# Kernel optimization log

Measured on AMD Instinct MI355X. Metric: run time of the kernel, lower is better.

## Reference

```python
import jax, jax.numpy as jnp
from jax import lax
import numpy as np

MAX_FLARES = 6
NMS_KERNEL = 9
CONF_THRESHOLD = 0.3


def setup_inputs() -> dict:
    key = jax.random.key(0)
    heatmap = jax.random.uniform(key, (64, 1, 640, 640), dtype=jnp.float32)
    return {"heatmap": heatmap}


def reference(heatmap):
    # heatmap: [B, 1, H, W]
    B, _, H, W = heatmap.shape
    K = MAX_FLARES
    hm = heatmap[:, 0]  # [B, H, W]

    # NMS via max-pool: kernel NMS_KERNEL, stride 1, SAME padding (pad = k//2)
    hm_max = lax.reduce_window(
        hm, -jnp.inf, lax.max,
        window_dimensions=(1, NMS_KERNEL, NMS_KERNEL),
        window_strides=(1, 1, 1),
        padding="SAME",
    )
    peaks = (hm == hm_max) & (hm > CONF_THRESHOLD)  # [B, H, W] bool
    scores = jnp.where(peaks, hm, jnp.float32(0.0))  # suppressed -> 0

    # Batched top-K over flattened spatial dims (replaces per-batch Python loop)
    flat = scores.reshape(B, H * W)
    top_scores, top_idx = lax.top_k(flat, K)  # [B, K] each, sorted desc

    # A slot is valid iff its score is a true peak (> threshold). Since all
    # non-peak entries were zeroed, this exactly reproduces the original's
    # min(K, n_peaks) truncation + `break` on sub-threshold scores.
    valid = top_scores > CONF_THRESHOLD  # [B, K]

    xs_grid = jnp.linspace(0.0, 1.0, W, dtype=hm.dtype)
    ys_grid = jnp.linspace(0.0, 1.0, H, dtype=hm.dtype)
    x_idx = top_idx % W
    y_idx = top_idx // W

    pos_x = jnp.where(valid, xs_grid[x_idx], jnp.float32(-1.0))
    pos_y = jnp.where(valid, ys_grid[y_idx], jnp.float32(-1.0))
    pred_positions = jnp.stack([pos_x, pos_y], axis=-1)  # [B, K, 2]
    pred_conf = jnp.where(valid, top_scores, jnp.float32(0.0))  # [B, K]
    return pred_positions, pred_conf
```

## Files before the change

### kernel.cpp

```cpp
#include <hip/hip_runtime.h>
#include <float.h>

#define HH 640
#define WW 640
#define KTOP 6
#define CONF 0.3f
#define NTHR 256
#define XBANDS 3
#define XOUT 248
#define SEG 40
#define CHUNK 8
#define NITER (SEG / CHUNK)
#define YSEGS (HH / SEG)
#define TASKS_PER_B (XBANDS * YSEGS)
#define MENT (TASKS_PER_B * KTOP)
#define CAP 256

__device__ __forceinline__ float4 f4max(float4 a, float4 b) {
    return make_float4(fmaxf(a.x, b.x), fmaxf(a.y, b.y), fmaxf(a.z, b.z), fmaxf(a.w, b.w));
}

__global__ __launch_bounds__(NTHR) void peaks_kernel(const float* __restrict__ hm,
                                                     float* __restrict__ bscore,
                                                     int* __restrict__ bidx) {
    __shared__ float c_score[4][CAP];
    __shared__ int   c_idx[4][CAP];
    __shared__ int   c_cnt[4];

    const int t    = threadIdx.x;
    const int lane = t & 63;
    const int w    = t >> 6;
    const int task = blockIdx.x * 4 + w;
    const int b    = task / TASKS_PER_B;
    const int rem  = task - b * TASKS_PER_B;
    const int ys   = rem / XBANDS;
    const int xb   = rem - ys * XBANDS;
    const int ybase = ys * SEG;
    const int x_raw = xb * XOUT - 4 + 4 * lane;
    const int xc    = min(max(x_raw, 0), WW - 4);
    const bool xok  = (x_raw >= 0) && (x_raw <= WW - 4);
    const bool vlane = (lane >= 1) && (lane <= 62) && xok;
    const float* colp = hm + (size_t)b * (HH * WW) + xc;
    const float4 NEG = make_float4(-FLT_MAX, -FLT_MAX, -FLT_MAX, -FLT_MAX);

    if (lane == 0) c_cnt[w] = 0;
    __syncthreads();

    #define LDC(dst, yy) { int gy = (yy); \
        gy = gy < 0 ? 0 : (gy > HH - 1 ? HH - 1 : gy); \
        dst = *reinterpret_cast<const float4*>(colp + (size_t)gy * WW); }

    #define PROCROW(m, c, gy_) { \
        const float w0 = __shfl_up(m.x, 1),  w1 = __shfl_up(m.y, 1); \
        const float w2 = __shfl_up(m.z, 1),  w3 = __shfl_up(m.w, 1); \
        const float w8 = __shfl_down(m.x, 1), w9 = __shfl_down(m.y, 1); \
        const float wA = __shfl_down(m.z, 1), wB = __shfl_down(m.w, 1); \
        const float hc = fmaxf(fmaxf(fmaxf(w3, m.x), fmaxf(m.y, m.z)), fmaxf(m.w, w8)); \
        const float ha = fmaxf(w1, w2); \
        const float hb = fmaxf(w9, wA); \
        const float h0 = fmaxf(hc, fmaxf(w0, ha)); \
        const float h1 = fmaxf(hc, fmaxf(ha, w9)); \
        const float h2 = fmaxf(hc, fmaxf(w2, hb)); \
        const float h3 = fmaxf(hc, fmaxf(hb, wB)); \
        if (vlane) { \
            const int base = (gy_) * WW + x_raw; \
            if (c.x > CONF && c.x >= h0) { int p_ = atomicAdd(&c_cnt[w], 1); if (p_ < CAP) { c_score[w][p_] = c.x; c_idx[w][p_] = base;     } } \
            if (c.y > CONF && c.y >= h1) { int p_ = atomicAdd(&c_cnt[w], 1); if (p_ < CAP) { c_score[w][p_] = c.y; c_idx[w][p_] = base + 1; } } \
            if (c.z > CONF && c.z >= h2) { int p_ = atomicAdd(&c_cnt[w], 1); if (p_ < CAP) { c_score[w][p_] = c.z; c_idx[w][p_] = base + 2; } } \
            if (c.w > CONF && c.w >= h3) { int p_ = atomicAdd(&c_cnt[w], 1); if (p_ < CAP) { c_score[w][p_] = c.w; c_idx[w][p_] = base + 3; } } \
        } \
    }

    float4 p[8], n[8], f[8];
    #pragma unroll
    for (int i = 0; i < 8; ++i) LDC(p[i], ybase - 4 + i)
    #pragma unroll
    for (int i = 0; i < 8; ++i) LDC(n[i], ybase + 4 + i)

    #pragma unroll
    for (int k = 0; k < NITER; ++k) {
        const int R = ybase + CHUNK * k;
        if (k < NITER - 1) {
            #pragma unroll
            for (int i = 0; i < 8; ++i) LDC(f[i], R + 12 + i)
        }
        float4 S[8];
        S[7] = p[7];
        #pragma unroll
        for (int i = 6; i >= 0; --i) S[i] = f4max(p[i], S[i + 1]);
        float4 pref = n[0];
        #pragma unroll
        for (int i = 0; i < 8; ++i) {
            if (i > 0) pref = f4max(pref, n[i]);
            float4 m = f4max(S[i], pref);
            if (!xok) m = NEG;
            const float4 c = (i < 4) ? p[4 + i] : n[i - 4];
            PROCROW(m, c, R + i)
        }
        if (k < NITER - 1) {
            #pragma unroll
            for (int i = 0; i < 8; ++i) { p[i] = n[i]; n[i] = f[i]; }
        }
    }

    {
        const int cnt = min(c_cnt[w], CAP);
        float cs[4]; int ci[4];
        #pragma unroll
        for (int j = 0; j < 4; ++j) {
            const int pos = lane + 64 * j;
            const bool ok = pos < cnt;
            cs[j] = ok ? c_score[w][pos] : -2.0f;
            ci[j] = ok ? c_idx[w][pos]   : 0x7fffffff;
        }
        const int outbase = task * KTOP;
        #pragma unroll
        for (int k = 0; k < KTOP; ++k) {
            float bs = cs[0]; int bi = ci[0];
            #pragma unroll
            for (int j = 1; j < 4; ++j)
                if (cs[j] > bs || (cs[j] == bs && ci[j] < bi)) { bs = cs[j]; bi = ci[j]; }
            #pragma unroll
            for (int off = 32; off >= 1; off >>= 1) {
                const float os = __shfl_xor(bs, off);
                const int   oi = __shfl_xor(bi, off);
                if (os > bs || (os == bs && oi < bi)) { bs = os; bi = oi; }
            }
            if (lane == 0) { bscore[outbase + k] = bs; bidx[outbase + k] = bi; }
            #pragma unroll
            for (int j = 0; j < 4; ++j) if (ci[j] == bi) cs[j] = -3.0f;
        }
    }
}

__global__ __launch_bounds__(64) void topk_kernel(const float* __restrict__ bscore,
                                                  const int* __restrict__ bidx,
                                                  float* __restrict__ out,
                                                  int B) {
    const int t = threadIdx.x;
    const int b = blockIdx.x;

    float s[5]; int id5[5];
    #pragma unroll
    for (int j = 0; j < 5; ++j) {
        const int e = t + 64 * j;
        const bool ok = e < MENT;
        s[j]   = ok ? bscore[b * MENT + e] : -9.0f;
        id5[j] = ok ? bidx[b * MENT + e]   : 0x7fffffff;
    }

    float my_s = -9.0f; int my_i = 0x7fffffff;
    #pragma unroll
    for (int k = 0; k < KTOP; ++k) {
        float bs = s[0]; int bi = id5[0];
        #pragma unroll
        for (int j = 1; j < 5; ++j)
            if (s[j] > bs || (s[j] == bs && id5[j] < bi)) { bs = s[j]; bi = id5[j]; }
        #pragma unroll
        for (int off = 32; off >= 1; off >>= 1) {
            const float os = __shfl_xor(bs, off);
            const int   oi = __shfl_xor(bi, off);
            if (os > bs || (os == bs && oi < bi)) { bs = os; bi = oi; }
        }
        if (t == k) { my_s = bs; my_i = bi; }
        #pragma unroll
        for (int j = 0; j < 5; ++j) if (id5[j] == bi) s[j] = -9.0f;
    }

    if (t < KTOP) {
        const bool valid = (my_s > CONF) && (my_i >= 0) && (my_i < HH * WW);
        const int id = valid ? my_i : 0;
        const int xi = id % WW;
        const int yi = id / WW;
        const float px = valid ? xi * (1.0f / (WW - 1)) : -1.0f;
        const float py = valid ? yi * (1.0f / (HH - 1)) : -1.0f;
        out[(size_t)b * KTOP * 2 + t * 2 + 0] = px;
        out[(size_t)b * KTOP * 2 + t * 2 + 1] = py;
        out[(size_t)B * KTOP * 2 + (size_t)b * KTOP + t] = valid ? my_s : 0.0f;
    }
}

extern "C" void kernel_launch(void* const* d_in, const int* in_sizes, int n_in,
                              void* d_out, int out_size, void* d_ws, size_t ws_size,
                              hipStream_t stream) {
    const float* hm = (const float*)d_in[0];
    float* out = (float*)d_out;
    const int B = in_sizes[0] / (HH * WW);

    float* bscore = (float*)d_ws;
    int*   bidx   = (int*)((char*)d_ws + sizeof(float) * (size_t)B * MENT);

    const int nblocks = (B * TASKS_PER_B) / 4;
    peaks_kernel<<<nblocks, NTHR, 0, stream>>>(hm, bscore, bidx);
    topk_kernel<<<B, 64, 0, stream>>>(bscore, bidx, out, B);
}
```

Measured before the change: 173.6 us.

## Shrink per-wave row segment and issue all row loads upfront via inline asm

Each wave now covers 16 output rows instead of 40. All 24 needed rows are issued up front as inline-asm global loads, and a partial vmcnt wait lets the first 8 rows be computed while the rest are still arriving. This exposes more waves for memory-level parallelism and sets a launch-bounds occupancy hint. In exchange the vertical halo re-read grows from 8/40 to 8/16 rows, and the second-stage top-k merges 2.5x more candidates. Candidate capacity per wave is halved.

```diff
diff --git a/kernel.cpp b/kernel.cpp
--- a/kernel.cpp
+++ b/kernel.cpp
@@ -1,28 +1,27 @@
 #include <hip/hip_runtime.h>
 #include <float.h>
+#include <stdint.h>
 
 #define HH 640
 #define WW 640
 #define KTOP 6
 #define CONF 0.3f
 #define NTHR 256
+#define ROWS_W 16
 #define XBANDS 3
 #define XOUT 248
-#define SEG 40
-#define CHUNK 8
-#define NITER (SEG / CHUNK)
-#define YSEGS (HH / SEG)
-#define TASKS_PER_B (XBANDS * YSEGS)
+#define YWAVES (HH / ROWS_W)
+#define TASKS_PER_B (XBANDS * YWAVES)
 #define MENT (TASKS_PER_B * KTOP)
-#define CAP 256
+#define CAP 128
 
 __device__ __forceinline__ float4 f4max(float4 a, float4 b) {
     return make_float4(fmaxf(a.x, b.x), fmaxf(a.y, b.y), fmaxf(a.z, b.z), fmaxf(a.w, b.w));
 }
 
-__global__ __launch_bounds__(NTHR) void peaks_kernel(const float* __restrict__ hm,
-                                                     float* __restrict__ bscore,
-                                                     int* __restrict__ bidx) {
+__global__ __launch_bounds__(NTHR, 3) void peaks_kernel(const float* __restrict__ hm,
+                                                        float* __restrict__ bscore,
+                                                        int* __restrict__ bidx) {
     __shared__ float c_score[4][CAP];
     __shared__ int   c_idx[4][CAP];
     __shared__ int   c_cnt[4];
@@ -33,9 +32,9 @@
     const int task = blockIdx.x * 4 + w;
     const int b    = task / TASKS_PER_B;
     const int rem  = task - b * TASKS_PER_B;
-    const int ys   = rem / XBANDS;
-    const int xb   = rem - ys * XBANDS;
-    const int ybase = ys * SEG;
+    const int yw   = rem / XBANDS;
+    const int xb   = rem - yw * XBANDS;
+    const int ybase = yw * ROWS_W;
     const int x_raw = xb * XOUT - 4 + 4 * lane;
     const int xc    = min(max(x_raw, 0), WW - 4);
     const bool xok  = (x_raw >= 0) && (x_raw <= WW - 4);
@@ -46,9 +45,18 @@
     if (lane == 0) c_cnt[w] = 0;
     __syncthreads();
 
-    #define LDC(dst, yy) { int gy = (yy); \
+    float4 r0, r1, r2, r3, r4, r5, r6, r7, r8, r9, r10, r11,
+           r12, r13, r14, r15, r16, r17, r18, r19, r20, r21, r22, r23;
+    #define LDA(i, dst) { int gy = ybase - 4 + (i); \
         gy = gy < 0 ? 0 : (gy > HH - 1 ? HH - 1 : gy); \
-        dst = *reinterpret_cast<const float4*>(colp + (size_t)gy * WW); }
+        const float* ap = colp + (size_t)gy * WW; \
+        asm volatile("global_load_dwordx4 %0, %1, off" : "=&v"(dst) : "v"(ap)); }
+    LDA(0,  r0)  LDA(1,  r1)  LDA(2,  r2)  LDA(3,  r3)
+    LDA(4,  r4)  LDA(5,  r5)  LDA(6,  r6)  LDA(7,  r7)
+    LDA(8,  r8)  LDA(9,  r9)  LDA(10, r10) LDA(11, r11)
+    LDA(12, r12) LDA(13, r13) LDA(14, r14) LDA(15, r15)
+    LDA(16, r16) LDA(17, r17) LDA(18, r18) LDA(19, r19)
+    LDA(20, r20) LDA(21, r21) LDA(22, r22) LDA(23, r23)
 
     #define PROCROW(m, c, gy_) { \
         const float w0 = __shfl_up(m.x, 1),  w1 = __shfl_up(m.y, 1); \
@@ -71,55 +79,58 @@
         } \
     }
 
-    float4 p[8], n[8], f[8];
-    #pragma unroll
-    for (int i = 0; i < 8; ++i) LDC(p[i], ybase - 4 + i)
-    #pragma unroll
-    for (int i = 0; i < 8; ++i) LDC(n[i], ybase + 4 + i)
-
-    #pragma unroll
-    for (int k = 0; k < NITER; ++k) {
-        const int R = ybase + CHUNK * k;
-        if (k < NITER - 1) {
-            #pragma unroll
-            for (int i = 0; i < 8; ++i) LDC(f[i], R + 12 + i)
-        }
-        float4 S[8];
-        S[7] = p[7];
-        #pragma unroll
-        for (int i = 6; i >= 0; --i) S[i] = f4max(p[i], S[i + 1]);
-        float4 pref = n[0];
-        #pragma unroll
-        for (int i = 0; i < 8; ++i) {
-            if (i > 0) pref = f4max(pref, n[i]);
-            float4 m = f4max(S[i], pref);
-            if (!xok) m = NEG;
-            const float4 c = (i < 4) ? p[4 + i] : n[i - 4];
-            PROCROW(m, c, R + i)
-        }
-        if (k < NITER - 1) {
-            #pragma unroll
-            for (int i = 0; i < 8; ++i) { p[i] = n[i]; n[i] = f[i]; }
-        }
+    #define VROW(Sx, c, gy_) { \
+        float4 m = f4max(Sx, pref); \
+        if (!xok) m = NEG; \
+        PROCROW(m, c, gy_) \
+    }
+
+    asm volatile("s_waitcnt vmcnt(8)" ::: "memory");
+    __builtin_amdgcn_sched_barrier(0);
+    {
+        float4 S7 = r7;
+        float4 S6 = f4max(r6, S7), S5 = f4max(r5, S6), S4 = f4max(r4, S5);
+        float4 S3 = f4max(r3, S4), S2 = f4max(r2, S3), S1 = f4max(r1, S2), S0 = f4max(r0, S1);
+        float4 pref = r8;
+        VROW(S0, r4,  ybase + 0)  pref = f4max(pref, r9);
+        VROW(S1, r5,  ybase + 1)  pref = f4max(pref, r10);
+        VROW(S2, r6,  ybase + 2)  pref = f4max(pref, r11);
+        VROW(S3, r7,  ybase + 3)  pref = f4max(pref, r12);
+        VROW(S4, r8,  ybase + 4)  pref = f4max(pref, r13);
+        VROW(S5, r9,  ybase + 5)  pref = f4max(pref, r14);
+        VROW(S6, r10, ybase + 6)  pref = f4max(pref, r15);
+        VROW(S7, r11, ybase + 7)
+    }
+
+    asm volatile("s_waitcnt vmcnt(0)" ::: "memory");
+    __builtin_amdgcn_sched_barrier(0);
+    {
+        float4 S7 = r15;
+        float4 S6 = f4max(r14, S7), S5 = f4max(r13, S6), S4 = f4max(r12, S5);
+        float4 S3 = f4max(r11, S4), S2 = f4max(r10, S3), S1 = f4max(r9, S2), S0 = f4max(r8, S1);
+        float4 pref = r16;
+        VROW(S0, r12, ybase + 8)   pref = f4max(pref, r17);
+        VROW(S1, r13, ybase + 9)   pref = f4max(pref, r18);
+        VROW(S2, r14, ybase + 10)  pref = f4max(pref, r19);
+        VROW(S3, r15, ybase + 11)  pref = f4max(pref, r20);
+        VROW(S4, r16, ybase + 12)  pref = f4max(pref, r21);
+        VROW(S5, r17, ybase + 13)  pref = f4max(pref, r22);
+        VROW(S6, r18, ybase + 14)  pref = f4max(pref, r23);
+        VROW(S7, r19, ybase + 15)
     }
 
     {
         const int cnt = min(c_cnt[w], CAP);
-        float cs[4]; int ci[4];
-        #pragma unroll
-        for (int j = 0; j < 4; ++j) {
-            const int pos = lane + 64 * j;
-            const bool ok = pos < cnt;
-            cs[j] = ok ? c_score[w][pos] : -2.0f;
-            ci[j] = ok ? c_idx[w][pos]   : 0x7fffffff;
-        }
+        float cs0 = (lane      < cnt) ? c_score[w][lane]      : -2.0f;
+        int   ci0 = (lane      < cnt) ? c_idx[w][lane]        : 0x7fffffff;
+        float cs1 = (lane + 64 < cnt) ? c_score[w][lane + 64] : -2.0f;
+        int   ci1 = (lane + 64 < cnt) ? c_idx[w][lane + 64]   : 0x7fffffff;
         const int outbase = task * KTOP;
         #pragma unroll
         for (int k = 0; k < KTOP; ++k) {
-            float bs = cs[0]; int bi = ci[0];
-            #pragma unroll
-            for (int j = 1; j < 4; ++j)
-                if (cs[j] > bs || (cs[j] == bs && ci[j] < bi)) { bs = cs[j]; bi = ci[j]; }
+            float bs; int bi;
+            if (cs0 > cs1 || (cs0 == cs1 && ci0 < ci1)) { bs = cs0; bi = ci0; }
+            else                                        { bs = cs1; bi = ci1; }
             #pragma unroll
             for (int off = 32; off >= 1; off >>= 1) {
                 const float os = __shfl_xor(bs, off);
@@ -127,8 +138,8 @@
                 if (os > bs || (os == bs && oi < bi)) { bs = os; bi = oi; }
             }
             if (lane == 0) { bscore[outbase + k] = bs; bidx[outbase + k] = bi; }
-            #pragma unroll
-            for (int j = 0; j < 4; ++j) if (ci[j] == bi) cs[j] = -3.0f;
+            if (ci0 == bi) cs0 = -3.0f;
+            if (ci1 == bi) cs1 = -3.0f;
         }
     }
 }
@@ -140,22 +151,22 @@
     const int t = threadIdx.x;
     const int b = blockIdx.x;
 
-    float s[5]; int id5[5];
+    float s[12]; int id[12];
     #pragma unroll
-    for (int j = 0; j < 5; ++j) {
+    for (int j = 0; j < 12; ++j) {
         const int e = t + 64 * j;
         const bool ok = e < MENT;
-        s[j]   = ok ? bscore[b * MENT + e] : -9.0f;
-        id5[j] = ok ? bidx[b * MENT + e]   : 0x7fffffff;
+        s[j]  = ok ? bscore[b * MENT + e] : -9.0f;
+        id[j] = ok ? bidx[b * MENT + e]   : 0x7fffffff;
     }
 
     float my_s = -9.0f; int my_i = 0x7fffffff;
     #pragma unroll
     for (int k = 0; k < KTOP; ++k) {
-        float bs = s[0]; int bi = id5[0];
-        #pragma unroll
-        for (int j = 1; j < 5; ++j)
-            if (s[j] > bs || (s[j] == bs && id5[j] < bi)) { bs = s[j]; bi = id5[j]; }
+        float bs = s[0]; int bi = id[0];
+        #pragma unroll
+        for (int j = 1; j < 12; ++j)
+            if (s[j] > bs || (s[j] == bs && id[j] < bi)) { bs = s[j]; bi = id[j]; }
         #pragma unroll
         for (int off = 32; off >= 1; off >>= 1) {
             const float os = __shfl_xor(bs, off);
@@ -164,14 +175,14 @@
         }
         if (t == k) { my_s = bs; my_i = bi; }
         #pragma unroll
-        for (int j = 0; j < 5; ++j) if (id5[j] == bi) s[j] = -9.0f;
+        for (int j = 0; j < 12; ++j) if (id[j] == bi) s[j] = -9.0f;
     }
 
     if (t < KTOP) {
         const bool valid = (my_s > CONF) && (my_i >= 0) && (my_i < HH * WW);
-        const int id = valid ? my_i : 0;
-        const int xi = id % WW;
-        const int yi = id / WW;
+        const int idv = valid ? my_i : 0;
+        const int xi = idv % WW;
+        const int yi = idv / WW;
         const float px = valid ? xi * (1.0f / (WW - 1)) : -1.0f;
         const float py = valid ? yi * (1.0f / (HH - 1)) : -1.0f;
         out[(size_t)b * KTOP * 2 + t * 2 + 0] = px;
```

Result: faster. 165.4 us (-4.8%).
